# Performance work log

Measured on AMD Instinct MI355X. Metric: run time of the kernel, lower is better.

Reference implementation:

```python
import jax, jax.numpy as jnp
import numpy as np

B, S, IN_DIM, HID = 8, 2048, 1024, 1024


def setup_inputs() -> dict:
    key = jax.random.key(0)
    k1, k2, k3, k4, k5 = jax.random.split(key, 5)
    vec = jax.random.normal(k1, (B, S, IN_DIM), dtype=jnp.float32)
    # nn.Linear-style init scale
    wq_w = jax.random.normal(k2, (HID, IN_DIM), dtype=jnp.float32) / np.sqrt(IN_DIM)
    wq_b = jax.random.normal(k3, (HID,), dtype=jnp.float32) * 0.02
    lin_w = jax.random.normal(k4, (1, HID), dtype=jnp.float32) / np.sqrt(HID)
    lin_b = jax.random.normal(k5, (1,), dtype=jnp.float32) * 0.02
    return {"vec": vec, "wq_w": wq_w, "wq_b": wq_b, "lin_w": lin_w, "lin_b": lin_b}


def reference(vec, wq_w, wq_b, lin_w, lin_b):
    # NOTE: the original forward applies self.wq to BOTH q and k (wk/nq/nk unused).
    q = jnp.einsum('bsi,hi->bsh', vec, wq_w) + wq_b          # [B,S,H]
    ret = jnp.einsum('bsx,bsy->bxy', q, q)                    # [B,H,H] bilinear
    ret = jax.nn.relu(ret)
    out = jnp.einsum('bxy,y->bx', ret, lin_w[0]) + lin_b[0]   # Linear(H,1) -> [B,H]
    return out
```

## Files before the change

### kernel.cpp

```cpp
#include <hip/hip_runtime.h>


typedef short     bf16x8 __attribute__((ext_vector_type(8)));
typedef unsigned short u16x8 __attribute__((ext_vector_type(8)));
typedef float     f32x4 __attribute__((ext_vector_type(4)));
typedef long long i64;

#define FENCE asm volatile("" ::: "memory")
#define BARR  do { FENCE; __builtin_amdgcn_s_barrier(); FENCE; } while (0)
#define VMCNT(N) asm volatile("s_waitcnt vmcnt(" #N ")" ::: "memory")

__device__ inline unsigned short f2bf(float f) {
  unsigned int u = __float_as_uint(f);
  u += 0x7fffu + ((u >> 16) & 1u);
  return (unsigned short)(u >> 16);
}

__device__ inline u16x8 pack8(float4 a, float4 b) {
  u16x8 r;
  r[0] = f2bf(a.x); r[1] = f2bf(a.y); r[2] = f2bf(a.z); r[3] = f2bf(a.w);
  r[4] = f2bf(b.x); r[5] = f2bf(b.y); r[6] = f2bf(b.z); r[7] = f2bf(b.w);
  return r;
}

__device__ inline unsigned char f2fp8(float v) {
  int pk = __builtin_amdgcn_cvt_pk_fp8_f32(v, v, 0, false);
  return (unsigned char)(pk & 0xff);
}

__device__ inline void async16(void* lds, const void* g) {
  __builtin_amdgcn_global_load_lds(
      (const __attribute__((address_space(1))) void*)g,
      (__attribute__((address_space(3))) void*)lds,
      16, 0, 0);
}

__global__ __launch_bounds__(256) void prep(
    const float* __restrict__ vec, unsigned short* __restrict__ vecbf,
    const float* __restrict__ wq,  unsigned short* __restrict__ wqbf,
    const float* __restrict__ lin_b, float* __restrict__ out)
{
  const int gid = blockIdx.x * 256 + threadIdx.x;
  if (blockIdx.x < 8192) {
    const float4* s = (const float4*)(vec + (size_t)gid * 8);
    float4 a = s[0], b = s[1];
    *(u16x8*)(vecbf + (size_t)gid * 8) = pack8(a, b);
    if (gid < 8192) out[gid] = lin_b[0];
  } else {
    const int i = gid - 8192 * 256;
    const float4* s = (const float4*)(wq + (size_t)i * 8);
    float4 a = s[0], b = s[1];
    *(u16x8*)(wqbf + (size_t)i * 8) = pack8(a, b);
  }
}

__global__ void init_out(float* __restrict__ out, const float* __restrict__ lin_b) {
  int i = blockIdx.x * 256 + threadIdx.x;
  if (i < 8192) out[i] = lin_b[0];
}

__global__ __launch_bounds__(512, 2) void gemm_q8p(
    const unsigned short* __restrict__ A, const unsigned short* __restrict__ Bm,
    const float* __restrict__ bias, unsigned char* __restrict__ qT8)
{
  __shared__ unsigned short As[2][256 * 64];
  __shared__ unsigned short Bs[2][256 * 64];

  const int m0 = blockIdx.y * 256;
  const int n0 = blockIdx.x * 256;
  const int t    = threadIdx.x;
  const int lane = t & 63;
  const int wave = t >> 6;
  const int wm2  = (wave >> 2) * 64;
  const int wn2  = (wave & 3) * 32;
  const int quad = lane >> 4;
  const int lrow = lane & 15;

  const int srow = t >> 3;
  const int gch  = (t & 7) ^ (srow & 7);
  const unsigned short* gA = A  + (size_t)(m0 + srow) * 1024 + gch * 8;
  const unsigned short* gB = Bm + (size_t)(n0 + srow) * 1024 + gch * 8;

#define STAGE_A(SLOT, H, KT) do { \
  _Pragma("unroll") for (int p = 0; p < 2; ++p) \
    async16(&As[SLOT][((H)*128 + p*64)*64 + t*8], \
            gA + (size_t)((H)*128 + p*64)*1024 + (KT)*64); \
} while (0)

#define STAGE_B(SLOT, H, KT) do { \
  _Pragma("unroll") for (int p = 0; p < 2; ++p) \
    async16(&Bs[SLOT][((H)*128 + p*64)*64 + t*8], \
            gB + (size_t)((H)*128 + p*64)*1024 + (KT)*64); \
} while (0)

#define LDA_HALF(S, MH) do { \
  _Pragma("unroll") for (int f = 0; f < 4; ++f) \
  _Pragma("unroll") for (int kk = 0; kk < 2; ++kk) \
    a_[f][kk] = *(const bf16x8*)&As[S][((MH)*128 + wm2 + f*16 + lrow)*64 + \
                                       (((kk*4 + quad) ^ (lrow & 7)) * 8)]; \
} while (0)

#define LDB_HALF(S, NH, BREG) do { \
  _Pragma("unroll") for (int g = 0; g < 2; ++g) \
  _Pragma("unroll") for (int kk = 0; kk < 2; ++kk) \
    BREG[g][kk] = *(const bf16x8*)&Bs[S][((NH)*128 + wn2 + g*16 + lrow)*64 + \
                                         (((kk*4 + quad) ^ (lrow & 7)) * 8)]; \
} while (0)

#define MFMAQ(MH, NH, BREG) do { \
  __builtin_amdgcn_s_setprio(1); \
  _Pragma("unroll") for (int kk = 0; kk < 2; ++kk) \
  _Pragma("unroll") for (int f = 0; f < 4; ++f) \
  _Pragma("unroll") for (int g = 0; g < 2; ++g) \
    acc[MH][f][NH][g] = __builtin_amdgcn_mfma_f32_16x16x32_bf16( \
        a_[f][kk], BREG[g][kk], acc[MH][f][NH][g], 0, 0, 0); \
  __builtin_amdgcn_s_setprio(0); \
} while (0)

  f32x4 acc[2][4][2][2];
#pragma unroll
  for (int i = 0; i < 2; ++i)
#pragma unroll
    for (int f = 0; f < 4; ++f)
#pragma unroll
      for (int j = 0; j < 2; ++j)
#pragma unroll
        for (int g = 0; g < 2; ++g) acc[i][f][j][g] = (f32x4){0.f, 0.f, 0.f, 0.f};

  bf16x8 a_[4][2], b0_[2][2], b1_[2][2];

  STAGE_A(0, 0, 0);
  STAGE_B(0, 0, 0);
  STAGE_B(0, 1, 0);
  STAGE_A(0, 1, 0);

#pragma unroll 1
  for (int kt = 0; kt < 15; ++kt) {
    const int s  = kt & 1;
    const int so = s ^ 1;

    STAGE_A(so, 0, kt + 1);
    STAGE_B(so, 0, kt + 1);
    VMCNT(8);
    BARR;
    LDA_HALF(s, 0);
    LDB_HALF(s, 0, b0_);
    MFMAQ(0, 0, b0_);
    BARR;

    STAGE_B(so, 1, kt + 1);
    VMCNT(8);
    BARR;
    LDB_HALF(s, 1, b1_);
    MFMAQ(0, 1, b1_);
    BARR;

    STAGE_A(so, 1, kt + 1);
    VMCNT(8);
    BARR;
    LDA_HALF(s, 1);
    MFMAQ(1, 0, b0_);
    MFMAQ(1, 1, b1_);
    BARR;
  }

  VMCNT(4);
  BARR;
  LDA_HALF(1, 0);
  LDB_HALF(1, 0, b0_);
  MFMAQ(0, 0, b0_);

  VMCNT(2);
  BARR;
  LDB_HALF(1, 1, b1_);
  MFMAQ(0, 1, b1_);

  VMCNT(0);
  BARR;
  LDA_HALF(1, 1);
  MFMAQ(1, 0, b0_);
  MFMAQ(1, 1, b1_);

#pragma unroll
  for (int mh = 0; mh < 2; ++mh)
#pragma unroll
    for (int f = 0; f < 4; ++f)
#pragma unroll
      for (int r = 0; r < 4; ++r) {
        const int m = m0 + mh * 128 + wm2 + f * 16 + quad * 4 + r;
        const float bv = bias[m];
        unsigned char* row = qT8 + (size_t)m * 16384 + n0;
#pragma unroll
        for (int nh = 0; nh < 2; ++nh)
#pragma unroll
          for (int g = 0; g < 2; ++g)
            row[nh * 128 + wn2 + g * 16 + lrow] = f2fp8(acc[mh][f][nh][g][r] + bv);
      }

#undef STAGE_A
#undef STAGE_B
#undef LDA_HALF
#undef LDB_HALF
#undef MFMAQ
}

__global__ __launch_bounds__(256) void gemm_q_fused(
    const float* __restrict__ Wq, const float* __restrict__ V,
    const float* __restrict__ bias, unsigned char* __restrict__ qT8)
{
  __shared__ unsigned short As[128 * 32];
  __shared__ unsigned short Bs[128 * 32];

  const int m0 = blockIdx.y * 128;
  const int n0 = blockIdx.x * 128;
  const int t    = threadIdx.x;
  const int lane = t & 63;
  const int wave = t >> 6;
  const int wm = (wave >> 1) * 64;
  const int wn = (wave & 1) * 64;
  const int quad = lane >> 4;
  const int lrow = lane & 15;

  const int sr = t >> 1;
  const int sc = (t & 1) << 4;
  const float* gA = Wq + (size_t)(m0 + sr) * 1024 + sc;
  const float* gB = V  + (size_t)(n0 + sr) * 1024 + sc;

  f32x4 acc[4][4];
#pragma unroll
  for (int i = 0; i < 4; ++i)
#pragma unroll
    for (int j = 0; j < 4; ++j) acc[i][j] = (f32x4){0.f, 0.f, 0.f, 0.f};

  for (int k0 = 0; k0 < 1024; k0 += 32) {
    const float4* a4 = (const float4*)(gA + k0);
    const float4* b4 = (const float4*)(gB + k0);
    float4 av0 = a4[0], av1 = a4[1], av2 = a4[2], av3 = a4[3];
    float4 bv0 = b4[0], bv1 = b4[1], bv2 = b4[2], bv3 = b4[3];
    *(u16x8*)&As[sr * 32 + sc]     = pack8(av0, av1);
    *(u16x8*)&As[sr * 32 + sc + 8] = pack8(av2, av3);
    *(u16x8*)&Bs[sr * 32 + sc]     = pack8(bv0, bv1);
    *(u16x8*)&Bs[sr * 32 + sc + 8] = pack8(bv2, bv3);
    __syncthreads();

    bf16x8 af[4], bfr[4];
#pragma unroll
    for (int i = 0; i < 4; ++i)
      af[i] = *(const bf16x8*)&As[(wm + i * 16 + lrow) * 32 + quad * 8];
#pragma unroll
    for (int j = 0; j < 4; ++j)
      bfr[j] = *(const bf16x8*)&Bs[(wn + j * 16 + lrow) * 32 + quad * 8];
#pragma unroll
    for (int i = 0; i < 4; ++i)
#pragma unroll
      for (int j = 0; j < 4; ++j)
        acc[i][j] = __builtin_amdgcn_mfma_f32_16x16x32_bf16(af[i], bfr[j], acc[i][j], 0, 0, 0);
    __syncthreads();
  }

#pragma unroll
  for (int i = 0; i < 4; ++i) {
    const int mb = m0 + wm + i * 16 + quad * 4;
#pragma unroll
    for (int r = 0; r < 4; ++r) {
      const float bv = bias[mb + r];
#pragma unroll
      for (int j = 0; j < 4; ++j) {
        const int n = n0 + wn + j * 16 + lrow;
        qT8[(size_t)(mb + r) * 16384 + n] = f2fp8(acc[i][j][r] + bv);
      }
    }
  }
}

__global__ __launch_bounds__(256) void syrk_half8(
    const unsigned char* __restrict__ qT8, const float* __restrict__ W,
    float* __restrict__ out)
{
  __shared__ unsigned char As[2][128 * 128];
  __shared__ unsigned char Bs[2][64 * 128];

  const int bb   = blockIdx.z;
  const int pair = blockIdx.x >> 1;
  const int yh   = blockIdx.x & 1;
  int tx = 0;
  while ((tx + 1) * (tx + 2) / 2 <= pair) ++tx;
  const int ty = pair - tx * (tx + 1) / 2;
  const int x0 = tx * 128;
  const int y0 = ty * 128 + yh * 64;
  const bool diag = (tx == ty);

  const int t    = threadIdx.x;
  const int lane = t & 63;
  const int wave = t >> 6;
  const int wm = (wave >> 1) * 64;
  const int wn = (wave & 1) * 32;
  const int quad = lane >> 4;
  const int lrow = lane & 15;

  const int srow = t >> 3;
  const int g16  = (t & 7) ^ (srow & 7);
  const size_t cb = (size_t)bb * 2048 + g16 * 16;
  const unsigned char* gA = qT8 + (size_t)(x0 + srow) * 16384 + cb;
  const unsigned char* gB = qT8 + (size_t)(y0 + srow) * 16384 + cb;

#define SSTAGE(SLOT, KT) do { \
  _Pragma("unroll") for (int p = 0; p < 4; ++p) \
    async16(&As[SLOT][p * 4096 + t * 16], gA + (size_t)p * 32 * 16384 + (KT) * 128); \
  _Pragma("unroll") for (int p = 0; p < 2; ++p) \
    async16(&Bs[SLOT][p * 4096 + t * 16], gB + (size_t)p * 32 * 16384 + (KT) * 128); \
} while (0)

#define SYRK_COMPUTE(S) do { \
  _Pragma("unroll") for (int kk = 0; kk < 4; ++kk) { \
    const int c = kk * 4 + quad; \
    const int off = (((c >> 1) ^ (lrow & 7)) << 4) + (c & 1) * 8; \
    i64 af[4], bfr[2]; \
    _Pragma("unroll") for (int i = 0; i < 4; ++i) \
      af[i] = *(const i64*)&As[S][(wm + i * 16 + lrow) * 128 + off]; \
    _Pragma("unroll") for (int j = 0; j < 2; ++j) \
      bfr[j] = *(const i64*)&Bs[S][(wn + j * 16 + lrow) * 128 + off]; \
    _Pragma("unroll") for (int i = 0; i < 4; ++i) \
      _Pragma("unroll") for (int j = 0; j < 2; ++j) \
        acc[i][j] = __builtin_amdgcn_mfma_f32_16x16x32_fp8_fp8(af[i], bfr[j], acc[i][j], 0, 0, 0); \
  } \
} while (0)

  f32x4 acc[4][2];
#pragma unroll
  for (int i = 0; i < 4; ++i)
#pragma unroll
    for (int j = 0; j < 2; ++j) acc[i][j] = (f32x4){0.f, 0.f, 0.f, 0.f};

  SSTAGE(0, 0);

#pragma unroll 1
  for (int kt = 0; kt < 15; ++kt) {
    const int s = kt & 1;
    SSTAGE(s ^ 1, kt + 1);
    VMCNT(6);
    BARR;
    SYRK_COMPUTE(s);
    BARR;
  }

  VMCNT(0);
  BARR;
  SYRK_COMPUTE(1);

#undef SSTAGE
#undef SYRK_COMPUTE

  float* ob = out + bb * 1024;

  float wv[2];
#pragma unroll
  for (int j = 0; j < 2; ++j) wv[j] = W[y0 + wn + j * 16 + lrow];

#pragma unroll
  for (int i = 0; i < 4; ++i) {
#pragma unroll
    for (int r = 0; r < 4; ++r) {
      float p = 0.f;
#pragma unroll
      for (int j = 0; j < 2; ++j) {
        float v = acc[i][j][r];
        v = v > 0.f ? v : 0.f;
        p += v * wv[j];
      }
#pragma unroll
      for (int off = 1; off < 16; off <<= 1) p += __shfl_xor(p, off, 64);
      if (lrow == 0)
        atomicAdd(&ob[x0 + wm + i * 16 + quad * 4 + r], p);
    }
  }

  if (!diag) {
    float wx[4][4];
#pragma unroll
    for (int i = 0; i < 4; ++i)
#pragma unroll
      for (int r = 0; r < 4; ++r)
        wx[i][r] = W[x0 + wm + i * 16 + quad * 4 + r];

#pragma unroll
    for (int j = 0; j < 2; ++j) {
      float pc = 0.f;
#pragma unroll
      for (int i = 0; i < 4; ++i)
#pragma unroll
        for (int r = 0; r < 4; ++r) {
          float v = acc[i][j][r];
          v = v > 0.f ? v : 0.f;
          pc += v * wx[i][r];
        }
      pc += __shfl_xor(pc, 16, 64);
      pc += __shfl_xor(pc, 32, 64);
      if (quad == 0)
        atomicAdd(&ob[y0 + wn + j * 16 + lrow], pc);
    }
  }
}

extern "C" void kernel_launch(void* const* d_in, const int* in_sizes, int n_in,
                              void* d_out, int out_size, void* d_ws, size_t ws_size,
                              hipStream_t stream) {
  const float* vec   = (const float*)d_in[0];
  const float* wq_w  = (const float*)d_in[1];
  const float* wq_b  = (const float*)d_in[2];
  const float* lin_w = (const float*)d_in[3];
  const float* lin_b = (const float*)d_in[4];
  float* out = (float*)d_out;

  unsigned char* qT8 = (unsigned char*)d_ws;
  const size_t need = (size_t)(16 + 32 + 2) * 1024 * 1024;

  if (ws_size >= need) {
    unsigned short* vecbf = (unsigned short*)((char*)d_ws + (size_t)16 * 1024 * 1024);
    unsigned short* wqbf  = vecbf + (size_t)16 * 1024 * 1024;
    prep<<<dim3(8192 + 512), dim3(256), 0, stream>>>(vec, vecbf, wq_w, wqbf, lin_b, out);
    gemm_q8p<<<dim3(64, 4), dim3(512), 0, stream>>>(wqbf, vecbf, wq_b, qT8);
  } else {
    init_out<<<dim3(32), dim3(256), 0, stream>>>(out, lin_b);
    gemm_q_fused<<<dim3(128, 8), dim3(256), 0, stream>>>(wq_w, vec, wq_b, qT8);
  }
  syrk_half8<<<dim3(72, 1, 8), dim3(256), 0, stream>>>(qT8, lin_w, out);
}
```

Before: 171.5 us.

## Triple-buffer B via async LDS loads and stage A through registers in GEMM

The projection GEMM now keeps three LDS slots for the B tile, filled with async global-to-LDS copies. The A tile goes through a register double-buffer and is written into a single LDS buffer after each compute step. The per-k-step barriers drop from six to two, giving the loads a deeper prefetch distance, at the cost of more registers and LDS. The SYRK kernel launch is also flattened to a 1-D grid with the batch index in the low bits, which changes how blocks interleave across CUs and cache.

```diff
diff --git a/kernel.cpp b/kernel.cpp
--- a/kernel.cpp
+++ b/kernel.cpp
@@ -9,6 +9,7 @@
 #define FENCE asm volatile("" ::: "memory")
 #define BARR  do { FENCE; __builtin_amdgcn_s_barrier(); FENCE; } while (0)
 #define VMCNT(N) asm volatile("s_waitcnt vmcnt(" #N ")" ::: "memory")
+#define LGKM0 asm volatile("s_waitcnt lgkmcnt(0)" ::: "memory")
 
 __device__ inline unsigned short f2bf(float f) {
   unsigned int u = __float_as_uint(f);
@@ -59,12 +60,12 @@
   if (i < 8192) out[i] = lin_b[0];
 }
 
-__global__ __launch_bounds__(512, 2) void gemm_q8p(
+__global__ __launch_bounds__(512, 2) void gemm_q3(
     const unsigned short* __restrict__ A, const unsigned short* __restrict__ Bm,
     const float* __restrict__ bias, unsigned char* __restrict__ qT8)
 {
-  __shared__ unsigned short As[2][256 * 64];
-  __shared__ unsigned short Bs[2][256 * 64];
+  __shared__ unsigned short As[256 * 64];
+  __shared__ unsigned short Bs[3][256 * 64];
 
   const int m0 = blockIdx.y * 256;
   const int n0 = blockIdx.x * 256;
@@ -78,26 +79,31 @@
 
   const int srow = t >> 3;
   const int gch  = (t & 7) ^ (srow & 7);
+  const int lsl  = srow * 64 + (t & 7) * 8;
   const unsigned short* gA = A  + (size_t)(m0 + srow) * 1024 + gch * 8;
   const unsigned short* gB = Bm + (size_t)(n0 + srow) * 1024 + gch * 8;
 
-#define STAGE_A(SLOT, H, KT) do { \
-  _Pragma("unroll") for (int p = 0; p < 2; ++p) \
-    async16(&As[SLOT][((H)*128 + p*64)*64 + t*8], \
-            gA + (size_t)((H)*128 + p*64)*1024 + (KT)*64); \
-} while (0)
-
-#define STAGE_B(SLOT, H, KT) do { \
-  _Pragma("unroll") for (int p = 0; p < 2; ++p) \
-    async16(&Bs[SLOT][((H)*128 + p*64)*64 + t*8], \
-            gB + (size_t)((H)*128 + p*64)*1024 + (KT)*64); \
-} while (0)
-
-#define LDA_HALF(S, MH) do { \
+#define STAGE_B3(SLOT, KT) do { \
+  _Pragma("unroll") for (int p = 0; p < 4; ++p) \
+    async16(&Bs[SLOT][p * 4096 + lsl], gB + (size_t)p * 65536 + (KT) * 64); \
+} while (0)
+
+#define LOAD_A3(RB, KT) do { \
+  _Pragma("unroll") for (int p = 0; p < 4; ++p) \
+    RB[p] = *reinterpret_cast<const uint4*>(gA + (size_t)p * 65536 + (KT) * 64); \
+} while (0)
+
+#define WRITE_A3(RB) do { \
+  _Pragma("unroll") for (int p = 0; p < 4; ++p) \
+    *reinterpret_cast<uint4*>(&As[p * 4096 + lsl]) = RB[p]; \
+  LGKM0; \
+} while (0)
+
+#define LDA_HALF(MH) do { \
   _Pragma("unroll") for (int f = 0; f < 4; ++f) \
   _Pragma("unroll") for (int kk = 0; kk < 2; ++kk) \
-    a_[f][kk] = *(const bf16x8*)&As[S][((MH)*128 + wm2 + f*16 + lrow)*64 + \
-                                       (((kk*4 + quad) ^ (lrow & 7)) * 8)]; \
+    a_[f][kk] = *(const bf16x8*)&As[((MH)*128 + wm2 + f*16 + lrow)*64 + \
+                                    (((kk*4 + quad) ^ (lrow & 7)) * 8)]; \
 } while (0)
 
 #define LDB_HALF(S, NH, BREG) do { \
@@ -117,6 +123,17 @@
   __builtin_amdgcn_s_setprio(0); \
 } while (0)
 
+#define COMPUTE(S) do { \
+  LDA_HALF(0); \
+  LDB_HALF(S, 0, b0_); \
+  MFMAQ(0, 0, b0_); \
+  LDB_HALF(S, 1, b1_); \
+  MFMAQ(0, 1, b1_); \
+  LDA_HALF(1); \
+  MFMAQ(1, 0, b0_); \
+  MFMAQ(1, 1, b1_); \
+} while (0)
+
   f32x4 acc[2][4][2][2];
 #pragma unroll
   for (int i = 0; i < 2; ++i)
@@ -128,58 +145,50 @@
         for (int g = 0; g < 2; ++g) acc[i][f][j][g] = (f32x4){0.f, 0.f, 0.f, 0.f};
 
   bf16x8 a_[4][2], b0_[2][2], b1_[2][2];
-
-  STAGE_A(0, 0, 0);
-  STAGE_B(0, 0, 0);
-  STAGE_B(0, 1, 0);
-  STAGE_A(0, 1, 0);
-
+  uint4 ra0[4], ra1[4];
+
+  LOAD_A3(ra0, 0);
+  STAGE_B3(0, 0);
+  LOAD_A3(ra1, 1);
+  STAGE_B3(1, 1);
+  VMCNT(12);
+  WRITE_A3(ra0);
+
+  int srd = 0;
+  int snx = 2;
 #pragma unroll 1
-  for (int kt = 0; kt < 15; ++kt) {
-    const int s  = kt & 1;
-    const int so = s ^ 1;
-
-    STAGE_A(so, 0, kt + 1);
-    STAGE_B(so, 0, kt + 1);
-    VMCNT(8);
-    BARR;
-    LDA_HALF(s, 0);
-    LDB_HALF(s, 0, b0_);
-    MFMAQ(0, 0, b0_);
-    BARR;
-
-    STAGE_B(so, 1, kt + 1);
-    VMCNT(8);
-    BARR;
-    LDB_HALF(s, 1, b1_);
-    MFMAQ(0, 1, b1_);
-    BARR;
-
-    STAGE_A(so, 1, kt + 1);
-    VMCNT(8);
-    BARR;
-    LDA_HALF(s, 1);
-    MFMAQ(1, 0, b0_);
-    MFMAQ(1, 1, b1_);
-    BARR;
+  for (int kt = 0; kt < 14; kt += 2) {
+    LOAD_A3(ra0, kt + 2);
+    STAGE_B3(snx, kt + 2);
+    VMCNT(12);
+    BARR;
+    COMPUTE(srd);
+    BARR;
+    WRITE_A3(ra1);
+    srd = (srd == 2) ? 0 : srd + 1;
+    snx = (snx == 2) ? 0 : snx + 1;
+
+    LOAD_A3(ra1, kt + 3);
+    STAGE_B3(snx, kt + 3);
+    VMCNT(12);
+    BARR;
+    COMPUTE(srd);
+    BARR;
+    WRITE_A3(ra0);
+    srd = (srd == 2) ? 0 : srd + 1;
+    snx = (snx == 2) ? 0 : snx + 1;
   }
 
   VMCNT(4);
   BARR;
-  LDA_HALF(1, 0);
-  LDB_HALF(1, 0, b0_);
-  MFMAQ(0, 0, b0_);
-
-  VMCNT(2);
+  COMPUTE(srd);
   BARR;
-  LDB_HALF(1, 1, b1_);
-  MFMAQ(0, 1, b1_);
+  WRITE_A3(ra1);
+  srd = (srd == 2) ? 0 : srd + 1;
 
   VMCNT(0);
   BARR;
-  LDA_HALF(1, 1);
-  MFMAQ(1, 0, b0_);
-  MFMAQ(1, 1, b1_);
+  COMPUTE(srd);
 
 #pragma unroll
   for (int mh = 0; mh < 2; ++mh)
@@ -197,11 +206,13 @@
             row[nh * 128 + wn2 + g * 16 + lrow] = f2fp8(acc[mh][f][nh][g][r] + bv);
       }
 
-#undef STAGE_A
-#undef STAGE_B
+#undef STAGE_B3
+#undef LOAD_A3
+#undef WRITE_A3
 #undef LDA_HALF
 #undef LDB_HALF
 #undef MFMAQ
+#undef COMPUTE
 }
 
 __global__ __launch_bounds__(256) void gemm_q_fused(
@@ -280,9 +291,10 @@
   __shared__ unsigned char As[2][128 * 128];
   __shared__ unsigned char Bs[2][64 * 128];
 
-  const int bb   = blockIdx.z;
-  const int pair = blockIdx.x >> 1;
-  const int yh   = blockIdx.x & 1;
+  const int bb   = blockIdx.x & 7;
+  const int id2  = blockIdx.x >> 3;
+  const int pair = id2 >> 1;
+  const int yh   = id2 & 1;
   int tx = 0;
   while ((tx + 1) * (tx + 2) / 2 <= pair) ++tx;
   const int ty = pair - tx * (tx + 1) / 2;
@@ -419,10 +431,10 @@
     unsigned short* vecbf = (unsigned short*)((char*)d_ws + (size_t)16 * 1024 * 1024);
     unsigned short* wqbf  = vecbf + (size_t)16 * 1024 * 1024;
     prep<<<dim3(8192 + 512), dim3(256), 0, stream>>>(vec, vecbf, wq_w, wqbf, lin_b, out);
-    gemm_q8p<<<dim3(64, 4), dim3(512), 0, stream>>>(wqbf, vecbf, wq_b, qT8);
+    gemm_q3<<<dim3(64, 4), dim3(512), 0, stream>>>(wqbf, vecbf, wq_b, qT8);
   } else {
     init_out<<<dim3(32), dim3(256), 0, stream>>>(out, lin_b);
     gemm_q_fused<<<dim3(128, 8), dim3(256), 0, stream>>>(wq_w, vec, wq_b, qT8);
   }
-  syrk_half8<<<dim3(72, 1, 8), dim3(256), 0, stream>>>(qT8, lin_w, out);
-}
+  syrk_half8<<<dim3(576), dim3(256), 0, stream>>>(qT8, lin_w, out);
+}
```

Measured after the change: 190.8 us. +11.2%, slower.
